# Performance work log

Measured on AMD Instinct MI355X. Metric: run time of the kernel, lower is better.

The kernel has to match this reference:

```python
import jax, jax.numpy as jnp
import numpy as np

EMBED = 1024
B, S = 4, 2048

def setup_inputs() -> dict:
    key = jax.random.key(0)
    k1, k2, k3, k4, k5, k6 = jax.random.split(key, 6)
    scale = 1.0 / np.sqrt(EMBED)
    return {
        "query": jax.random.normal(k1, (B, S, EMBED), dtype=jnp.float32),
        "key": jax.random.normal(k2, (B, S, EMBED), dtype=jnp.float32),
        "value": jax.random.normal(k3, (B, S, EMBED), dtype=jnp.float32),
        # nn.Linear weights, stored torch-style [out, in]; y = x @ W.T
        "Q_W": jax.random.normal(k4, (EMBED, EMBED), dtype=jnp.float32) * scale,
        "K_W": jax.random.normal(k5, (EMBED, EMBED), dtype=jnp.float32) * scale,
        "V_W": jax.random.normal(k6, (EMBED, EMBED), dtype=jnp.float32) * scale,
    }

def reference(query, key, value, Q_W, K_W, V_W):
    q = jnp.einsum('bse,oe->bso', query, Q_W)   # Linear(bias=False): x @ W.T
    k = jnp.einsum('bse,oe->bso', key, K_W)
    v = jnp.einsum('bse,oe->bso', value, V_W)
    scores = jnp.einsum('bqe,bke->bqk', q, k) / jnp.sqrt(jnp.asarray(q.shape[-1], q.dtype))
    attn = jax.nn.softmax(scores, axis=-1)      # [b, q, k]
    out = jnp.einsum('bqs,bse->bqe', attn, v)
    return out
```

## Files before the change

kernel.cpp:

```cpp
#include <hip/hip_runtime.h>
#include <stdint.h>


typedef __attribute__((ext_vector_type(8))) short short8;
typedef __attribute__((ext_vector_type(4))) float floatx4;
typedef __attribute__((ext_vector_type(4))) unsigned short u16x4;
typedef __attribute__((ext_vector_type(4))) float f32x4v;

__device__ __forceinline__ unsigned short f32_to_bf16(float f) {
    union { float f; unsigned u; } c; c.f = f;
    unsigned u = c.u;
    return (unsigned short)((u + 0x7fffu + ((u >> 16) & 1u)) >> 16);
}

#define G2L(g, l) __builtin_amdgcn_global_load_lds( \
    (__attribute__((address_space(1))) void*)(void*)(g), \
    (__attribute__((address_space(3))) void*)(l), 16, 0, 0)

#define BAR() __builtin_amdgcn_s_barrier()

__global__ __launch_bounds__(256) void cvt_all(
    const float* __restrict__ q, const float* __restrict__ k,
    const float* __restrict__ v, const float* __restrict__ wq,
    const float* __restrict__ wk, const float* __restrict__ wv,
    unsigned short* __restrict__ Xq, unsigned short* __restrict__ Xk,
    unsigned short* __restrict__ Xv, unsigned short* __restrict__ Wq,
    unsigned short* __restrict__ Wk, unsigned short* __restrict__ Wv,
    float* __restrict__ rowsum) {
    const long NTE4 = 2097152;
    const long NW4  = 262144;
    long i = (long)blockIdx.x * 256 + threadIdx.x;
    const float* src;
    unsigned short* dst;
    long j;
    if (i < 3 * NTE4) {
        int a = (int)(i / NTE4); j = i - (long)a * NTE4;
        src = a == 0 ? q : a == 1 ? k : v;
        dst = a == 0 ? Xq : a == 1 ? Xk : Xv;
    } else {
        i -= 3 * NTE4;
        if (i < 3 * NW4) {
            int a = (int)(i / NW4); j = i - (long)a * NW4;
            src = a == 0 ? wq : a == 1 ? wk : wv;
            dst = a == 0 ? Wq : a == 1 ? Wk : Wv;
        } else {
            i -= 3 * NW4;
            ((f32x4v*)rowsum)[i] = (f32x4v)0.0f;
            return;
        }
    }
    f32x4v f = ((const f32x4v*)src)[j];
    u16x4 o;
#pragma unroll
    for (int t = 0; t < 4; ++t) o[t] = f32_to_bf16(f[t]);
    ((u16x4*)dst)[j] = o;
}

#define BM 128
#define BN 128
#define BK 64

template <int EPI>
__device__ __forceinline__ void gemm_body(
    const unsigned short* __restrict__ A, const unsigned short* __restrict__ B,
    void* __restrict__ Cv, int lda, int ldb, int ldc, int K, float scale,
    float* __restrict__ rowsum, int m0, int n0) {
    __shared__ unsigned short As[BM * BK];
    __shared__ unsigned short Bs[BN * BK];

    const int tid  = threadIdx.x;
    const int wave = tid >> 6;
    const int lane = tid & 63;
    const int lm   = lane & 15;
    const int quad = lane >> 4;
    const int wm   = wave >> 1;
    const int wn   = wave & 1;

    const int srow8 = lane >> 3;
    const int gcol  = ((lane & 7) ^ srow8) * 8;

    floatx4 acc[4][4];
#pragma unroll
    for (int i = 0; i < 4; ++i)
#pragma unroll
        for (int j = 0; j < 4; ++j) acc[i][j] = (floatx4)0.0f;

    for (int k0 = 0; k0 < K; k0 += BK) {
#pragma unroll
        for (int i = 0; i < 4; ++i) {
            const int rbase = wave * 32 + i * 8;
            G2L(A + (size_t)(m0 + rbase + srow8) * lda + k0 + gcol,
                &As[rbase * BK]);
            G2L(B + (size_t)(n0 + rbase + srow8) * ldb + k0 + gcol,
                &Bs[rbase * BK]);
        }
        __syncthreads();

#pragma unroll
        for (int s = 0; s < 2; ++s) {
            short8 af[4], bf[4];
#pragma unroll
            for (int t = 0; t < 4; ++t) {
                const int cs = ((s * 4 + quad) ^ (lm & 7)) * 8;
                af[t] = *(const short8*)&As[(wm * 64 + t * 16 + lm) * BK + cs];
                bf[t] = *(const short8*)&Bs[(wn * 64 + t * 16 + lm) * BK + cs];
            }
#pragma unroll
            for (int mt = 0; mt < 4; ++mt)
#pragma unroll
                for (int nt = 0; nt < 4; ++nt)
                    acc[mt][nt] = __builtin_amdgcn_mfma_f32_16x16x32_bf16(
                        af[mt], bf[nt], acc[mt][nt], 0, 0, 0);
        }
        __syncthreads();
    }

    if constexpr (EPI == 0) {
        unsigned short* C = (unsigned short*)Cv;
#pragma unroll
        for (int mt = 0; mt < 4; ++mt)
#pragma unroll
            for (int nt = 0; nt < 4; ++nt)
#pragma unroll
                for (int r = 0; r < 4; ++r) {
                    const int row = m0 + wm * 64 + mt * 16 + quad * 4 + r;
                    const int col = n0 + wn * 64 + nt * 16 + lm;
                    C[(size_t)row * ldc + col] = f32_to_bf16(acc[mt][nt][r]);
                }
    } else if constexpr (EPI == 2) {
        float* C = (float*)Cv;
#pragma unroll
        for (int mt = 0; mt < 4; ++mt)
#pragma unroll
            for (int r = 0; r < 4; ++r) {
                const int row = m0 + wm * 64 + mt * 16 + quad * 4 + r;
                const float inv = 1.0f / rowsum[row];
#pragma unroll
                for (int nt = 0; nt < 4; ++nt) {
                    const int col = n0 + wn * 64 + nt * 16 + lm;
                    C[(size_t)row * ldc + col] = acc[mt][nt][r] * inv;
                }
            }
    }
}

__global__ __launch_bounds__(256, 4) void proj_kernel(
    const unsigned short* __restrict__ Xq, const unsigned short* __restrict__ Wq,
    unsigned short* __restrict__ qb,
    const unsigned short* __restrict__ Xk, const unsigned short* __restrict__ Wk,
    unsigned short* __restrict__ kb,
    const unsigned short* __restrict__ Wv, const unsigned short* __restrict__ Xv,
    unsigned short* __restrict__ vT) {
    const int z = blockIdx.z;
    const unsigned short* A = z == 0 ? Xq : z == 1 ? Xk : Wv;
    const unsigned short* B = z == 0 ? Wq : z == 1 ? Wk : Xv;
    unsigned short* C = z == 0 ? qb : z == 1 ? kb : vT;
    int m0, n0, ldc;
    if (z < 2) { m0 = blockIdx.x * BM; n0 = blockIdx.y * BN; ldc = 1024; }
    else       { m0 = blockIdx.y * BM; n0 = blockIdx.x * BN; ldc = 8192; }
    gemm_body<0>(A, B, C, 1024, 1024, ldc, 1024, 1.0f, nullptr, m0, n0);
}

__global__ __launch_bounds__(256, 4) void pv_kernel(
    const unsigned short* __restrict__ Sc, const unsigned short* __restrict__ vT,
    float* __restrict__ out, float* __restrict__ rowsum) {
    const long z = blockIdx.z;
    gemm_body<2>(Sc + z * 2048 * 2048, vT + z * 2048,
                 out + z * 2048 * 1024, 2048, 8192, 1024, 2048,
                 1.0f, rowsum + z * 2048,
                 blockIdx.x * BM, blockIdx.y * BN);
}

template <int EPI>
__device__ __forceinline__ void gemm256_body(
    const unsigned short* __restrict__ A, const unsigned short* __restrict__ B,
    void* __restrict__ Cv, int lda, int ldb, int ldc, int K, float scale,
    float* __restrict__ rowsum, int m0, int n0) {
    __shared__ unsigned short As[2][256 * 64];
    __shared__ unsigned short Bs[2][256 * 64];

    const int tid   = threadIdx.x;
    const int wave  = tid >> 6;
    const int lane  = tid & 63;
    const int lm    = lane & 15;
    const int quad  = lane >> 4;
    const int wm    = wave >> 2;
    const int wn    = wave & 3;
    const int srow8 = lane >> 3;
    const int gcol  = ((lane & 7) ^ srow8) * 8;
    const int KT    = K >> 6;

#define STAGE_A(buf, half, kcol) do { \
        const int r0_ = (half) * 128 + wave * 8; \
        G2L(A + (size_t)(m0 + r0_ + srow8) * lda + (kcol) + gcol, \
            &As[buf][r0_ * 64]); \
        G2L(A + (size_t)(m0 + r0_ + 64 + srow8) * lda + (kcol) + gcol, \
            &As[buf][(r0_ + 64) * 64]); \
    } while (0)
#define STAGE_B(buf, half, kcol) do { \
        const int r0_ = (half) * 128 + wave * 8; \
        G2L(B + (size_t)(n0 + r0_ + srow8) * ldb + (kcol) + gcol, \
            &Bs[buf][r0_ * 64]); \
        G2L(B + (size_t)(n0 + r0_ + 64 + srow8) * ldb + (kcol) + gcol, \
            &Bs[buf][(r0_ + 64) * 64]); \
    } while (0)

    floatx4 acc[8][4];
#pragma unroll
    for (int i = 0; i < 8; ++i)
#pragma unroll
        for (int j = 0; j < 4; ++j) acc[i][j] = (floatx4)0.0f;

    STAGE_A(0, 0, 0); STAGE_A(0, 1, 0); STAGE_B(0, 0, 0); STAGE_B(0, 1, 0);
    if (KT > 1) {
        STAGE_A(1, 0, 64); STAGE_A(1, 1, 64);
        STAGE_B(1, 0, 64); STAGE_B(1, 1, 64);
        asm volatile("s_waitcnt vmcnt(8)" ::: "memory");
    } else {
        asm volatile("s_waitcnt vmcnt(0)" ::: "memory");
    }
    BAR();

    short8 aA[2][4];
    short8 aM[2][4];
    short8 bB[2][2];

    for (int kt = 0; kt < KT; ++kt) {
        const int b = kt & 1;
        const unsigned short* Ab = As[b];
        const unsigned short* Bb = Bs[b];

#pragma unroll
        for (int s = 0; s < 2; ++s) {
            const int cs = ((s * 4 + quad) ^ (lm & 7)) * 8;
#pragma unroll
            for (int mt = 0; mt < 4; ++mt)
                aA[s][mt] = *(const short8*)&Ab[(wm * 128 + mt * 16 + lm) * 64 + cs];
#pragma unroll
            for (int nt = 0; nt < 2; ++nt)
                bB[s][nt] = *(const short8*)&Bb[(wn * 64 + nt * 16 + lm) * 64 + cs];
        }
#pragma unroll
        for (int s = 0; s < 2; ++s) {
            const int cs = ((s * 4 + quad) ^ (lm & 7)) * 8;
#pragma unroll
            for (int mt = 0; mt < 4; ++mt)
                aM[s][mt] = *(const short8*)&Ab[(wm * 128 + 64 + mt * 16 + lm) * 64 + cs];
        }
        BAR();
        __builtin_amdgcn_s_setprio(1);
#pragma unroll
        for (int s = 0; s < 2; ++s)
#pragma unroll
            for (int mt = 0; mt < 4; ++mt)
#pragma unroll
                for (int nt = 0; nt < 2; ++nt)
                    acc[mt][nt] = __builtin_amdgcn_mfma_f32_16x16x32_bf16(
                        aA[s][mt], bB[s][nt], acc[mt][nt], 0, 0, 0);
        __builtin_amdgcn_s_setprio(0);
        BAR();

        BAR();
        __builtin_amdgcn_s_setprio(1);
#pragma unroll
        for (int s = 0; s < 2; ++s)
#pragma unroll
            for (int mt = 0; mt < 4; ++mt)
#pragma unroll
                for (int nt = 0; nt < 2; ++nt)
                    acc[4 + mt][nt] = __builtin_amdgcn_mfma_f32_16x16x32_bf16(
                        aM[s][mt], bB[s][nt], acc[4 + mt][nt], 0, 0, 0);
        __builtin_amdgcn_s_setprio(0);
        BAR();

#pragma unroll
        for (int s = 0; s < 2; ++s) {
            const int cs = ((s * 4 + quad) ^ (lm & 7)) * 8;
#pragma unroll
            for (int nt = 0; nt < 2; ++nt)
                bB[s][nt] = *(const short8*)&Bb[(wn * 64 + 32 + nt * 16 + lm) * 64 + cs];
        }
        if (kt + 2 < KT) { STAGE_A(b, 0, (kt + 2) * 64); STAGE_A(b, 1, (kt + 2) * 64); }
        BAR();
        __builtin_amdgcn_s_setprio(1);
#pragma unroll
        for (int s = 0; s < 2; ++s)
#pragma unroll
            for (int mt = 0; mt < 4; ++mt)
#pragma unroll
                for (int nt = 0; nt < 2; ++nt)
                    acc[4 + mt][2 + nt] = __builtin_amdgcn_mfma_f32_16x16x32_bf16(
                        aM[s][mt], bB[s][nt], acc[4 + mt][2 + nt], 0, 0, 0);
        __builtin_amdgcn_s_setprio(0);
        BAR();

        if (kt + 2 < KT) { STAGE_B(b, 0, (kt + 2) * 64); STAGE_B(b, 1, (kt + 2) * 64); }
        BAR();
        __builtin_amdgcn_s_setprio(1);
#pragma unroll
        for (int s = 0; s < 2; ++s)
#pragma unroll
            for (int mt = 0; mt < 4; ++mt)
#pragma unroll
                for (int nt = 0; nt < 2; ++nt)
                    acc[mt][2 + nt] = __builtin_amdgcn_mfma_f32_16x16x32_bf16(
                        aA[s][mt], bB[s][nt], acc[mt][2 + nt], 0, 0, 0);
        __builtin_amdgcn_s_setprio(0);
        if (kt + 2 < KT) {
            asm volatile("s_waitcnt vmcnt(8)" ::: "memory");
        } else if (kt + 1 < KT) {
            asm volatile("s_waitcnt vmcnt(0)" ::: "memory");
        }
        BAR();
    }
#undef STAGE_A
#undef STAGE_B

    if constexpr (EPI == 1) {
        unsigned short* C = (unsigned short*)Cv;
        float psum[8][4];
#pragma unroll
        for (int f = 0; f < 8; ++f)
#pragma unroll
            for (int r = 0; r < 4; ++r) psum[f][r] = 0.0f;
#pragma unroll
        for (int f = 0; f < 8; ++f)
#pragma unroll
            for (int g = 0; g < 4; ++g)
#pragma unroll
                for (int r = 0; r < 4; ++r) {
                    const int row = m0 + wm * 128 + f * 16 + quad * 4 + r;
                    const int col = n0 + wn * 64 + g * 16 + lm;
                    const float p = __expf(acc[f][g][r] * scale);
                    psum[f][r] += p;
                    C[(size_t)row * ldc + col] = f32_to_bf16(p);
                }
#pragma unroll
        for (int off = 1; off <= 8; off <<= 1)
#pragma unroll
            for (int f = 0; f < 8; ++f)
#pragma unroll
                for (int r = 0; r < 4; ++r)
                    psum[f][r] += __shfl_xor(psum[f][r], off);
        if (lm == 0) {
#pragma unroll
            for (int f = 0; f < 8; ++f)
#pragma unroll
                for (int r = 0; r < 4; ++r)
                    atomicAdd(&rowsum[m0 + wm * 128 + f * 16 + quad * 4 + r],
                              psum[f][r]);
        }
    }
}

__global__ __launch_bounds__(512, 2) void scores256_kernel(
    const unsigned short* __restrict__ qb, const unsigned short* __restrict__ kb,
    unsigned short* __restrict__ Sc, float* __restrict__ rowsum) {
    const long z = blockIdx.z;
    gemm256_body<1>(qb + z * 2048 * 1024, kb + z * 2048 * 1024,
                    Sc + z * 2048 * 2048, 1024, 1024, 2048, 1024,
                    1.0f / 32.0f, rowsum + z * 2048,
                    blockIdx.x * 256, blockIdx.y * 256);
}

extern "C" void kernel_launch(void* const* d_in, const int* in_sizes, int n_in,
                              void* d_out, int out_size, void* d_ws, size_t ws_size,
                              hipStream_t stream) {
    const float* q_in = (const float*)d_in[0];
    const float* k_in = (const float*)d_in[1];
    const float* v_in = (const float*)d_in[2];
    const float* Qw_f = (const float*)d_in[3];
    const float* Kw_f = (const float*)d_in[4];
    const float* Vw_f = (const float*)d_in[5];
    float* out = (float*)d_out;

    const int Bb = 4, S = 2048, E = 1024;
    const size_t TOK = (size_t)Bb * S;
    const size_t NTE = TOK * E;
    const size_t NW  = (size_t)E * E;

    unsigned short* ws = (unsigned short*)d_ws;
    unsigned short* Xq = ws;
    unsigned short* Xk = Xq + NTE;
    unsigned short* Xv = Xk + NTE;
    unsigned short* Wq = Xv + NTE;
    unsigned short* Wk = Wq + NW;
    unsigned short* Wv = Wk + NW;
    unsigned short* qb = Wv + NW;
    unsigned short* kb = qb + NTE;
    unsigned short* vT = kb + NTE;
    unsigned short* Sc = vT + NTE;
    float* rowsum = (float*)(Sc + (size_t)Bb * S * S);

    {
        const long G = 3 * (long)(NTE / 4) + 3 * (long)(NW / 4) + (Bb * S / 4);
        cvt_all<<<(unsigned)(G / 256), 256, 0, stream>>>(
            q_in, k_in, v_in, Qw_f, Kw_f, Vw_f,
            Xq, Xk, Xv, Wq, Wk, Wv, rowsum);
    }

    proj_kernel<<<dim3(TOK / BM, E / BN, 3), 256, 0, stream>>>(
        Xq, Wq, qb, Xk, Wk, kb, Wv, Xv, vT);

    scores256_kernel<<<dim3(S / 256, S / 256, 4), 512, 0, stream>>>(
        qb, kb, Sc, rowsum);

    pv_kernel<<<dim3(S / BM, E / BN, 4), 256, 0, stream>>>(
        Sc, vT, out, rowsum);
}
```

Baseline: 289.9 us.

## Fold key projection into query weights via precomputed Wq^T·Wk product

Computes M = Wk^T-contracted product of the Q and K weight matrices (fp32 SIMT tiles inside the conversion kernel) and projects the query with it, so the scores GEMM uses the raw bf16 key directly. This removes the separate key projection GEMM and the Wq/Wk conversions, cutting one of three projection GEMMs. It adds a 1024^3 fp32 scalar matmul done by 1024 small blocks in the conversion launch and changes rounding, since the product is rounded to bf16 once.

```diff
diff --git a/kernel.cpp b/kernel.cpp
--- a/kernel.cpp
+++ b/kernel.cpp
@@ -6,6 +6,7 @@
 typedef __attribute__((ext_vector_type(4))) float floatx4;
 typedef __attribute__((ext_vector_type(4))) unsigned short u16x4;
 typedef __attribute__((ext_vector_type(4))) float f32x4v;
+typedef __attribute__((ext_vector_type(2))) float f32x2v;
 
 __device__ __forceinline__ unsigned short f32_to_bf16(float f) {
     union { float f; unsigned u; } c; c.f = f;
@@ -18,15 +19,51 @@
     (__attribute__((address_space(3))) void*)(l), 16, 0, 0)
 
 #define BAR() __builtin_amdgcn_s_barrier()
+
+#define CVT_BLOCKS 25608
 
 __global__ __launch_bounds__(256) void cvt_all(
     const float* __restrict__ q, const float* __restrict__ k,
     const float* __restrict__ v, const float* __restrict__ wq,
     const float* __restrict__ wk, const float* __restrict__ wv,
     unsigned short* __restrict__ Xq, unsigned short* __restrict__ Xk,
-    unsigned short* __restrict__ Xv, unsigned short* __restrict__ Wq,
-    unsigned short* __restrict__ Wk, unsigned short* __restrict__ Wv,
-    float* __restrict__ rowsum) {
+    unsigned short* __restrict__ Xv, unsigned short* __restrict__ Wv,
+    unsigned short* __restrict__ Mp, float* __restrict__ rowsum) {
+    __shared__ float Ao[32][36];
+    __shared__ float Bo[32][36];
+
+    if (blockIdx.x >= CVT_BLOCKS) {
+        const int id = blockIdx.x - CVT_BLOCKS;
+        const int t0 = (id >> 5) * 32;
+        const int k0 = (id & 31) * 32;
+        const int tx = threadIdx.x & 15;
+        const int ty = threadIdx.x >> 4;
+        const int sr = threadIdx.x >> 3;
+        const int sc = (threadIdx.x & 7) * 4;
+        float a00 = 0.f, a01 = 0.f, a10 = 0.f, a11 = 0.f;
+        for (int o0 = 0; o0 < 1024; o0 += 32) {
+            *(f32x4v*)&Ao[sr][sc] =
+                *(const f32x4v*)&wk[(size_t)(o0 + sr) * 1024 + t0 + sc];
+            *(f32x4v*)&Bo[sr][sc] =
+                *(const f32x4v*)&wq[(size_t)(o0 + sr) * 1024 + k0 + sc];
+            __syncthreads();
+#pragma unroll
+            for (int o = 0; o < 32; ++o) {
+                const f32x2v av = *(const f32x2v*)&Ao[o][tx * 2];
+                const f32x2v bv = *(const f32x2v*)&Bo[o][ty * 2];
+                a00 += av[0] * bv[0]; a01 += av[0] * bv[1];
+                a10 += av[1] * bv[0]; a11 += av[1] * bv[1];
+            }
+            __syncthreads();
+        }
+        const int t = t0 + tx * 2, kk = k0 + ty * 2;
+        Mp[(size_t)t * 1024 + kk]           = f32_to_bf16(a00);
+        Mp[(size_t)t * 1024 + kk + 1]       = f32_to_bf16(a01);
+        Mp[(size_t)(t + 1) * 1024 + kk]     = f32_to_bf16(a10);
+        Mp[(size_t)(t + 1) * 1024 + kk + 1] = f32_to_bf16(a11);
+        return;
+    }
+
     const long NTE4 = 2097152;
     const long NW4  = 262144;
     long i = (long)blockIdx.x * 256 + threadIdx.x;
@@ -39,13 +76,11 @@
         dst = a == 0 ? Xq : a == 1 ? Xk : Xv;
     } else {
         i -= 3 * NTE4;
-        if (i < 3 * NW4) {
-            int a = (int)(i / NW4); j = i - (long)a * NW4;
-            src = a == 0 ? wq : a == 1 ? wk : wv;
-            dst = a == 0 ? Wq : a == 1 ? Wk : Wv;
+        if (i < NW4) {
+            src = wv; dst = Wv; j = i;
         } else {
-            i -= 3 * NW4;
-            ((f32x4v*)rowsum)[i] = (f32x4v)0.0f;
+            i -= NW4;
+            if (i < 2048) ((f32x4v*)rowsum)[i] = (f32x4v)0.0f;
             return;
         }
     }
@@ -145,19 +180,17 @@
 }
 
 __global__ __launch_bounds__(256, 4) void proj_kernel(
-    const unsigned short* __restrict__ Xq, const unsigned short* __restrict__ Wq,
+    const unsigned short* __restrict__ Xq, const unsigned short* __restrict__ Mp,
     unsigned short* __restrict__ qb,
-    const unsigned short* __restrict__ Xk, const unsigned short* __restrict__ Wk,
-    unsigned short* __restrict__ kb,
     const unsigned short* __restrict__ Wv, const unsigned short* __restrict__ Xv,
     unsigned short* __restrict__ vT) {
     const int z = blockIdx.z;
-    const unsigned short* A = z == 0 ? Xq : z == 1 ? Xk : Wv;
-    const unsigned short* B = z == 0 ? Wq : z == 1 ? Wk : Xv;
-    unsigned short* C = z == 0 ? qb : z == 1 ? kb : vT;
+    const unsigned short* A = z == 0 ? Xq : Wv;
+    const unsigned short* B = z == 0 ? Mp : Xv;
+    unsigned short* C = z == 0 ? qb : vT;
     int m0, n0, ldc;
-    if (z < 2) { m0 = blockIdx.x * BM; n0 = blockIdx.y * BN; ldc = 1024; }
-    else       { m0 = blockIdx.y * BM; n0 = blockIdx.x * BN; ldc = 8192; }
+    if (z == 0) { m0 = blockIdx.x * BM; n0 = blockIdx.y * BN; ldc = 1024; }
+    else        { m0 = blockIdx.y * BM; n0 = blockIdx.x * BN; ldc = 8192; }
     gemm_body<0>(A, B, C, 1024, 1024, ldc, 1024, 1.0f, nullptr, m0, n0);
 }
 
@@ -354,10 +387,10 @@
 }
 
 __global__ __launch_bounds__(512, 2) void scores256_kernel(
-    const unsigned short* __restrict__ qb, const unsigned short* __restrict__ kb,
+    const unsigned short* __restrict__ qb, const unsigned short* __restrict__ Xk,
     unsigned short* __restrict__ Sc, float* __restrict__ rowsum) {
     const long z = blockIdx.z;
-    gemm256_body<1>(qb + z * 2048 * 1024, kb + z * 2048 * 1024,
+    gemm256_body<1>(qb + z * 2048 * 1024, Xk + z * 2048 * 1024,
                     Sc + z * 2048 * 2048, 1024, 1024, 2048, 1024,
                     1.0f / 32.0f, rowsum + z * 2048,
                     blockIdx.x * 256, blockIdx.y * 256);
@@ -383,27 +416,22 @@
     unsigned short* Xq = ws;
     unsigned short* Xk = Xq + NTE;
     unsigned short* Xv = Xk + NTE;
-    unsigned short* Wq = Xv + NTE;
-    unsigned short* Wk = Wq + NW;
-    unsigned short* Wv = Wk + NW;
-    unsigned short* qb = Wv + NW;
-    unsigned short* kb = qb + NTE;
-    unsigned short* vT = kb + NTE;
+    unsigned short* Wv = Xv + NTE;
+    unsigned short* Mp = Wv + NW;
+    unsigned short* qb = Mp + NW;
+    unsigned short* vT = qb + NTE;
     unsigned short* Sc = vT + NTE;
     float* rowsum = (float*)(Sc + (size_t)Bb * S * S);
 
-    {
-        const long G = 3 * (long)(NTE / 4) + 3 * (long)(NW / 4) + (Bb * S / 4);
-        cvt_all<<<(unsigned)(G / 256), 256, 0, stream>>>(
-            q_in, k_in, v_in, Qw_f, Kw_f, Vw_f,
-            Xq, Xk, Xv, Wq, Wk, Wv, rowsum);
-    }
-
-    proj_kernel<<<dim3(TOK / BM, E / BN, 3), 256, 0, stream>>>(
-        Xq, Wq, qb, Xk, Wk, kb, Wv, Xv, vT);
+    cvt_all<<<CVT_BLOCKS + 1024, 256, 0, stream>>>(
+        q_in, k_in, v_in, Qw_f, Kw_f, Vw_f,
+        Xq, Xk, Xv, Wv, Mp, rowsum);
+
+    proj_kernel<<<dim3(TOK / BM, E / BN, 2), 256, 0, stream>>>(
+        Xq, Mp, qb, Wv, Xv, vT);
 
     scores256_kernel<<<dim3(S / 256, S / 256, 4), 512, 0, stream>>>(
-        qb, kb, Sc, rowsum);
+        qb, Xk, Sc, rowsum);
 
     pv_kernel<<<dim3(S / BM, E / BN, 4), 256, 0, stream>>>(
         Sc, vT, out, rowsum);
```

Measured after the change: 401.0 us. 1.38x slower.
